# Kernel optimization log

Hardware: AMD Instinct MI355X
Metric: run time of the kernel (lower is better)

Reference implementation:

```python
import jax, jax.numpy as jnp
import numpy as np

N_CLASSES = 128
NAN_TO = 0.0


def setup_inputs() -> dict:
    key = jax.random.key(0)
    k1, k2 = jax.random.split(key)
    B, n = 500000, N_CLASSES
    y_hat = jax.random.normal(k1, (B, n), dtype=jnp.float32)
    y = jax.random.uniform(k2, (B, n), dtype=jnp.float32)
    return {"y_hat": y_hat, "y": y}


def reference(y_hat, y):
    # class id per sample (argmax over class dim)
    y_cls = jnp.argmax(y, axis=1)  # [B] int
    # per-sample loss (loss_fn with reduction='none'): soft-target cross entropy
    loss = -jnp.sum(y * jax.nn.log_softmax(y_hat, axis=-1), axis=1)  # [B]
    # per-class mean via a single-pass segment reduce (replaces the O(n*B) mask loop)
    seg_sum = jax.ops.segment_sum(loss, y_cls, num_segments=N_CLASSES)
    counts = jax.ops.segment_sum(jnp.ones_like(loss), y_cls, num_segments=N_CLASSES)
    # mean over an empty class would be NaN in torch; replaced by nan_to
    out = jnp.where(counts > 0, seg_sum / jnp.maximum(counts, 1.0), NAN_TO)
    return out
```

## Files before the change

### kernel.cpp

```cpp
#include <hip/hip_runtime.h>

#define N_CLASSES 128

__global__ __launch_bounds__(256, 8) void class_loss_kernel(
    const float* __restrict__ y_hat,
    const float* __restrict__ y,
    float* __restrict__ ws,
    int B)
{
    __shared__ float s_sum[N_CLASSES];
    __shared__ float s_cnt[N_CLASSES];
    const int tid = threadIdx.x;
    for (int i = tid; i < N_CLASSES; i += blockDim.x) { s_sum[i] = 0.f; s_cnt[i] = 0.f; }
    __syncthreads();

    const int lane    = tid & 15;
    const int group   = (blockIdx.x * blockDim.x + tid) >> 4;
    const int ngroups = (gridDim.x * blockDim.x) >> 4;

    const float4* __restrict__ ph = (const float4*)y_hat;
    const float4* __restrict__ pt = (const float4*)y;

    for (int row = group; row < B; row += ngroups) {
        const size_t base = (size_t)row * (N_CLASSES / 4);
        const float4 h0 = ph[base + lane];
        const float4 h1 = ph[base + lane + 16];
        const float4 t0 = pt[base + lane];
        const float4 t1 = pt[base + lane + 16];

        float m  = fmaxf(fmaxf(fmaxf(h0.x, h0.y), fmaxf(h0.z, h0.w)),
                         fmaxf(fmaxf(h1.x, h1.y), fmaxf(h1.z, h1.w)));
        float bv = fmaxf(fmaxf(fmaxf(t0.x, t0.y), fmaxf(t0.z, t0.w)),
                         fmaxf(fmaxf(t1.x, t1.y), fmaxf(t1.z, t1.w)));
        #pragma unroll
        for (int o = 8; o >= 1; o >>= 1) {
            m  = fmaxf(m,  __shfl_xor(m,  o));
            bv = fmaxf(bv, __shfl_xor(bv, o));
        }

        float s = __expf(h0.x - m) + __expf(h0.y - m) + __expf(h0.z - m) + __expf(h0.w - m)
                + __expf(h1.x - m) + __expf(h1.y - m) + __expf(h1.z - m) + __expf(h1.w - m);
        float dot = t0.x * h0.x + t0.y * h0.y + t0.z * h0.z + t0.w * h0.w
                  + t1.x * h1.x + t1.y * h1.y + t1.z * h1.z + t1.w * h1.w;
        float sy = (t0.x + t0.y + t0.z + t0.w) + (t1.x + t1.y + t1.z + t1.w);

        const int e0 = lane * 4, e1 = 64 + lane * 4;
        int bi = N_CLASSES;
        bi = (t1.w == bv) ? e1 + 3 : bi;
        bi = (t1.z == bv) ? e1 + 2 : bi;
        bi = (t1.y == bv) ? e1 + 1 : bi;
        bi = (t1.x == bv) ? e1     : bi;
        bi = (t0.w == bv) ? e0 + 3 : bi;
        bi = (t0.z == bv) ? e0 + 2 : bi;
        bi = (t0.y == bv) ? e0 + 1 : bi;
        bi = (t0.x == bv) ? e0     : bi;

        #pragma unroll
        for (int o = 8; o >= 1; o >>= 1) {
            s   += __shfl_xor(s,   o);
            dot += __shfl_xor(dot, o);
            sy  += __shfl_xor(sy,  o);
            bi   = min(bi, __shfl_xor(bi, o));
        }

        if (lane == 0) {
            float loss = (m + __logf(s)) * sy - dot;
            atomicAdd(&s_sum[bi], loss);
            atomicAdd(&s_cnt[bi], 1.0f);
        }
    }

    __syncthreads();
    for (int i = tid; i < N_CLASSES; i += blockDim.x) {
        if (s_cnt[i] > 0.f) {
            atomicAdd(&ws[i], s_sum[i]);
            atomicAdd(&ws[N_CLASSES + i], s_cnt[i]);
        }
    }
}

__global__ void finalize_kernel(const float* __restrict__ ws, float* __restrict__ out) {
    const int c = threadIdx.x;
    if (c < N_CLASSES) {
        float cnt = ws[N_CLASSES + c];
        out[c] = (cnt > 0.f) ? ws[c] / cnt : 0.0f;
    }
}

extern "C" void kernel_launch(void* const* d_in, const int* in_sizes, int n_in,
                              void* d_out, int out_size, void* d_ws, size_t ws_size,
                              hipStream_t stream) {
    const float* y_hat = (const float*)d_in[0];
    const float* y     = (const float*)d_in[1];
    float* ws  = (float*)d_ws;
    float* out = (float*)d_out;
    const int B = in_sizes[0] / N_CLASSES;

    hipMemsetAsync(d_ws, 0, 2 * N_CLASSES * sizeof(float), stream);

    const int blocks = 2048;
    class_loss_kernel<<<blocks, 256, 0, stream>>>(y_hat, y, ws, B);
    finalize_kernel<<<1, N_CLASSES, 0, stream>>>(ws, out);
}
```

Baseline: 489.7 us.

## Process each row with 4 lanes and 16 float4 loads per lane

Each row is now handled by 4 lanes instead of 16, with each lane loading eight float4 values from each input. This cuts the cross-lane shuffle reductions from four levels to two and puts more independent loads in flight per thread. It also lowers the occupancy hint in launch bounds to allow the higher register use. The trade-off is more registers per thread and fewer waves to hide memory latency. Coalescing stays the same, because adjacent groups of 4 lanes still cover contiguous 64-byte chunks.

```diff
diff --git a/kernel.cpp b/kernel.cpp
--- a/kernel.cpp
+++ b/kernel.cpp
@@ -2,7 +2,7 @@
 
 #define N_CLASSES 128
 
-__global__ __launch_bounds__(256, 8) void class_loss_kernel(
+__global__ __launch_bounds__(256, 4) void class_loss_kernel(
     const float* __restrict__ y_hat,
     const float* __restrict__ y,
     float* __restrict__ ws,
@@ -14,49 +14,55 @@
     for (int i = tid; i < N_CLASSES; i += blockDim.x) { s_sum[i] = 0.f; s_cnt[i] = 0.f; }
     __syncthreads();
 
-    const int lane    = tid & 15;
-    const int group   = (blockIdx.x * blockDim.x + tid) >> 4;
-    const int ngroups = (gridDim.x * blockDim.x) >> 4;
+    const int lane    = tid & 3;
+    const int group   = (blockIdx.x * blockDim.x + tid) >> 2;
+    const int ngroups = (gridDim.x * blockDim.x) >> 2;
 
     const float4* __restrict__ ph = (const float4*)y_hat;
     const float4* __restrict__ pt = (const float4*)y;
 
     for (int row = group; row < B; row += ngroups) {
-        const size_t base = (size_t)row * (N_CLASSES / 4);
-        const float4 h0 = ph[base + lane];
-        const float4 h1 = ph[base + lane + 16];
-        const float4 t0 = pt[base + lane];
-        const float4 t1 = pt[base + lane + 16];
+        const size_t base = (size_t)row * (N_CLASSES / 4) + lane;
 
-        float m  = fmaxf(fmaxf(fmaxf(h0.x, h0.y), fmaxf(h0.z, h0.w)),
-                         fmaxf(fmaxf(h1.x, h1.y), fmaxf(h1.z, h1.w)));
-        float bv = fmaxf(fmaxf(fmaxf(t0.x, t0.y), fmaxf(t0.z, t0.w)),
-                         fmaxf(fmaxf(t1.x, t1.y), fmaxf(t1.z, t1.w)));
+        float4 h[8], t[8];
         #pragma unroll
-        for (int o = 8; o >= 1; o >>= 1) {
-            m  = fmaxf(m,  __shfl_xor(m,  o));
-            bv = fmaxf(bv, __shfl_xor(bv, o));
+        for (int k = 0; k < 8; ++k) h[k] = ph[base + 4 * k];
+        #pragma unroll
+        for (int k = 0; k < 8; ++k) t[k] = pt[base + 4 * k];
+
+        float m = -INFINITY, bv = -INFINITY;
+        #pragma unroll
+        for (int k = 0; k < 8; ++k) {
+            m  = fmaxf(m,  fmaxf(fmaxf(h[k].x, h[k].y), fmaxf(h[k].z, h[k].w)));
+            bv = fmaxf(bv, fmaxf(fmaxf(t[k].x, t[k].y), fmaxf(t[k].z, t[k].w)));
+        }
+        m  = fmaxf(m,  __shfl_xor(m,  1));
+        m  = fmaxf(m,  __shfl_xor(m,  2));
+        bv = fmaxf(bv, __shfl_xor(bv, 1));
+        bv = fmaxf(bv, __shfl_xor(bv, 2));
+
+        float s = 0.f, dot = 0.f, sy = 0.f;
+        #pragma unroll
+        for (int k = 0; k < 8; ++k) {
+            s   += __expf(h[k].x - m) + __expf(h[k].y - m)
+                 + __expf(h[k].z - m) + __expf(h[k].w - m);
+            dot += t[k].x * h[k].x + t[k].y * h[k].y
+                 + t[k].z * h[k].z + t[k].w * h[k].w;
+            sy  += (t[k].x + t[k].y) + (t[k].z + t[k].w);
         }
 
-        float s = __expf(h0.x - m) + __expf(h0.y - m) + __expf(h0.z - m) + __expf(h0.w - m)
-                + __expf(h1.x - m) + __expf(h1.y - m) + __expf(h1.z - m) + __expf(h1.w - m);
-        float dot = t0.x * h0.x + t0.y * h0.y + t0.z * h0.z + t0.w * h0.w
-                  + t1.x * h1.x + t1.y * h1.y + t1.z * h1.z + t1.w * h1.w;
-        float sy = (t0.x + t0.y + t0.z + t0.w) + (t1.x + t1.y + t1.z + t1.w);
-
-        const int e0 = lane * 4, e1 = 64 + lane * 4;
         int bi = N_CLASSES;
-        bi = (t1.w == bv) ? e1 + 3 : bi;
-        bi = (t1.z == bv) ? e1 + 2 : bi;
-        bi = (t1.y == bv) ? e1 + 1 : bi;
-        bi = (t1.x == bv) ? e1     : bi;
-        bi = (t0.w == bv) ? e0 + 3 : bi;
-        bi = (t0.z == bv) ? e0 + 2 : bi;
-        bi = (t0.y == bv) ? e0 + 1 : bi;
-        bi = (t0.x == bv) ? e0     : bi;
+        #pragma unroll
+        for (int k = 7; k >= 0; --k) {
+            const int e = (lane + 4 * k) * 4;
+            if (t[k].w == bv) bi = e + 3;
+            if (t[k].z == bv) bi = e + 2;
+            if (t[k].y == bv) bi = e + 1;
+            if (t[k].x == bv) bi = e;
+        }
 
         #pragma unroll
-        for (int o = 8; o >= 1; o >>= 1) {
+        for (int o = 2; o >= 1; o >>= 1) {
             s   += __shfl_xor(s,   o);
             dot += __shfl_xor(dot, o);
             sy  += __shfl_xor(sy,  o);
```

New measurement: 488.8 us. About the same (-0.2%).
